# Optimization experiments

Measured on AMD Instinct MI355X. Metric: run time of the kernel, lower is better.

The kernel has to match this reference:

```python
import jax, jax.numpy as jnp
import numpy as np

# Config constants from init_kwargs
DIM_GROUPS = [32, 32]   # hyper_cuts_dim_groups (sum == lsh_key_dim == d_key)
K_MAX = 64              # max candidates kept per query token


def _group_exact_match(qb, kb):
    """qb, kb: [B, L, d] binary {0,1} floats.
    Returns eq[b, i, j] = True iff all d bits of query i equal key j.
    Faithful to merge(Wu-Manber prefix match, Trie full-stride match):
    the Trie stores the full binary vector chunked by stride, so a Trie hit
    requires exact equality of the whole group's bit vector, which subsumes
    the Wu-Manber prefix condition; their intersection is exact equality.
    """
    # number of mismatching bits between query i and key j
    mism = (jnp.einsum('bid,bjd->bij', qb, 1.0 - kb)
            + jnp.einsum('bid,bjd->bij', 1.0 - qb, kb))
    return mism == 0.0


def setup_inputs() -> dict:
    key = jax.random.key(0)
    k1, k2 = jax.random.split(key)
    B, L, D = 4, 2048, 64
    return {
        'query_up': jax.random.normal(k1, (B, L, D), dtype=jnp.float32),
        'key_up': jax.random.normal(k2, (B, L, D), dtype=jnp.float32),
        'head_idx': 0,
    }


def reference(query_up, key_up, head_idx):
    B, L, _ = query_up.shape
    # binary_quantize: (x > 0).float()
    qb = (query_up > 0).astype(jnp.float32)
    kb = (key_up > 0).astype(jnp.float32)
    # per dim-group exact match (Wu-Manber \cap Trie), union across groups
    match = jnp.zeros((B, L, L), dtype=bool)
    start = 0
    for gd in DIM_GROUPS:
        match = match | _group_exact_match(qb[..., start:start + gd],
                                           kb[..., start:start + gd])
        start += gd
    # gather up to K_MAX smallest matching key indices per query, pad with -1
    idx = jnp.where(match, jnp.arange(L, dtype=jnp.int32)[None, None, :], L)
    cand = jnp.sort(idx, axis=-1)[..., :K_MAX]          # [B, L, K_MAX]
    return jnp.where(cand == L, -1, cand)
```

## Files before the change

kernel.cpp:

```cpp
#include <hip/hip_runtime.h>
#include <stdint.h>


#define LSEQ 2048
#define DDIM 64
#define KMAX 64
#define RPW  8

__global__ __launch_bounds__(256) void sig_kernel(
    const float* __restrict__ key, uint2* __restrict__ ksig, int nrows) {
    int wid  = (int)((blockIdx.x * blockDim.x + threadIdx.x) >> 6);
    int lane = threadIdx.x & 63;
    int row0 = wid * RPW;
    if (row0 >= nrows) return;
    const float* base = key + (size_t)row0 * DDIM + lane;
    float v[RPW];
#pragma unroll
    for (int u = 0; u < RPW; ++u)
        v[u] = base[(size_t)u * DDIM];
    unsigned long long m[RPW];
#pragma unroll
    for (int u = 0; u < RPW; ++u)
        m[u] = __ballot(v[u] > 0.0f);
    if (lane == 0) {
#pragma unroll
        for (int u = 0; u < RPW; ++u)
            ksig[row0 + u] = make_uint2((unsigned)m[u], (unsigned)(m[u] >> 32));
    }
}

__global__ __launch_bounds__(256) void match_kernel(
    const float* __restrict__ query, const uint2* __restrict__ ksig,
    int* __restrict__ out, int nq) {
    int wid  = (int)((blockIdx.x * blockDim.x + threadIdx.x) >> 6);
    int lane = threadIdx.x & 63;
    int q0 = wid * 2;
    if (q0 >= nq) return;
    int b = q0 >> 11;

    const float* qp = query + (size_t)q0 * DDIM + lane;
    float v0 = qp[0], v1 = qp[DDIM];
    unsigned long long qm0 = __ballot(v0 > 0.0f);
    unsigned long long qm1 = __ballot(v1 > 0.0f);
    unsigned a0 = (unsigned)qm0, g0 = (unsigned)(qm0 >> 32);
    unsigned a1 = (unsigned)qm1, g1 = (unsigned)(qm1 >> 32);

    const uint4* kt = (const uint4*)(ksig + (size_t)b * LSEQ) + lane;
    unsigned long long acc0 = 0, acc1 = 0;
    int cnt0 = 0, cnt1 = 0;
#pragma unroll
    for (int i = 0; i < LSEQ / 128; ++i) {
        uint4 kv = kt[(size_t)i * 64];
        bool mA0 = (kv.x == a0) | (kv.y == g0);
        bool mB0 = (kv.z == a0) | (kv.w == g0);
        bool mA1 = (kv.x == a1) | (kv.y == g1);
        bool mB1 = (kv.z == a1) | (kv.w == g1);
        unsigned long long s;
        s = __ballot(mA0); acc0 |= s; cnt0 += __popcll(s);
        s = __ballot(mB0); acc0 |= s; cnt0 += __popcll(s);
        s = __ballot(mA1); acc1 |= s; cnt1 += __popcll(s);
        s = __ballot(mB1); acc1 |= s; cnt1 += __popcll(s);
    }

    int* o0 = out + (size_t)q0 * KMAX;
    int* o1 = o0 + KMAX;

    if (acc0 | acc1) {
        const uint2* ks = ksig + (size_t)b * LSEQ;
        unsigned long long below = (1ull << lane) - 1ull;
        for (int t = 0; t < 2; ++t) {
            unsigned qa = t ? a1 : a0, qg = t ? g1 : g0;
            int* ob = t ? o1 : o0;
            int c2 = 0;
            for (int c = 0; c < LSEQ / 64; ++c) {
                uint2 kv = ks[c * 64 + lane];
                bool m = (kv.x == qa) || (kv.y == qg);
                unsigned long long mask = __ballot(m);
                if (m) {
                    int pos = c2 + __popcll(mask & below);
                    if (pos < KMAX) ob[pos] = c * 64 + lane;
                }
                c2 += __popcll(mask);
            }
        }
    }
    if (lane >= cnt0) o0[lane] = -1;
    if (lane >= cnt1) o1[lane] = -1;
}

#define QPB  32
#define NW   16
#define GROUP 32
__global__ __launch_bounds__(1024) void fused_kernel(
    const float* __restrict__ query, const float* __restrict__ key,
    int* __restrict__ out) {
    __shared__ uint2 ks[LSEQ];
    const int bpb  = LSEQ / QPB;
    int b    = blockIdx.x / bpb;
    int qblk = blockIdx.x % bpb;
    int lane = threadIdx.x & 63;
    int wave = threadIdx.x >> 6;
    const float* kb = key + (size_t)b * LSEQ * DDIM;
    for (int g = 0; g < LSEQ / NW / GROUP; ++g) {
        float v[GROUP];
#pragma unroll
        for (int u = 0; u < GROUP; ++u)
            v[u] = kb[(size_t)(g * (NW * GROUP) + u * NW + wave) * DDIM + lane];
        unsigned long long m[GROUP];
#pragma unroll
        for (int u = 0; u < GROUP; ++u) m[u] = __ballot(v[u] > 0.0f);
        if (lane == 0) {
#pragma unroll
            for (int u = 0; u < GROUP; ++u)
                ks[g * (NW * GROUP) + u * NW + wave] =
                    make_uint2((unsigned)m[u], (unsigned)(m[u] >> 32));
        }
    }
    const float* qb = query + ((size_t)b * LSEQ + (size_t)qblk * QPB) * DDIM;
    int q0 = wave * 2;
    float v0 = qb[(size_t)q0 * DDIM + lane];
    float v1 = qb[(size_t)(q0 + 1) * DDIM + lane];
    unsigned long long m0 = __ballot(v0 > 0.0f);
    unsigned long long m1 = __ballot(v1 > 0.0f);
    __syncthreads();
    unsigned long long below = (1ull << lane) - 1ull;
    for (int t = 0; t < 2; ++t) {
        unsigned long long qm = t ? m1 : m0;
        unsigned q1 = (unsigned)qm, q2 = (unsigned)(qm >> 32);
        int* obase = out + ((size_t)b * LSEQ + (size_t)qblk * QPB + q0 + t) * KMAX;
        unsigned long long acc = 0;
        int cnt = 0;
#pragma unroll
        for (int c = 0; c < LSEQ / 64; ++c) {
            uint2 kv = ks[c * 64 + lane];
            bool m = (kv.x == q1) || (kv.y == q2);
            unsigned long long mask = __ballot(m);
            acc |= mask; cnt += __popcll(mask);
        }
        if (acc != 0) {
            int c2 = 0;
            for (int c = 0; c < LSEQ / 64; ++c) {
                uint2 kv = ks[c * 64 + lane];
                bool m = (kv.x == q1) || (kv.y == q2);
                unsigned long long mask = __ballot(m);
                if (m) {
                    int pos = c2 + __popcll(mask & below);
                    if (pos < KMAX) obase[pos] = c * 64 + lane;
                }
                c2 += __popcll(mask);
            }
        }
        if (lane >= cnt) obase[lane] = -1;
    }
}

extern "C" void kernel_launch(void* const* d_in, const int* in_sizes, int n_in,
                              void* d_out, int out_size, void* d_ws, size_t ws_size,
                              hipStream_t stream) {
    const float* q = (const float*)d_in[0];
    const float* k = (const float*)d_in[1];
    int* out = (int*)d_out;

    int total = in_sizes[0];
    int B = total / (LSEQ * DDIM);
    int nrows = B * LSEQ;

    if (ws_size >= (size_t)nrows * sizeof(uint2)) {
        uint2* ksig = (uint2*)d_ws;
        int sig_waves = nrows / RPW;
        sig_kernel<<<sig_waves * 64 / 256, 256, 0, stream>>>(k, ksig, nrows);
        int match_waves = nrows / 2;
        match_kernel<<<match_waves * 64 / 256, 256, 0, stream>>>(q, ksig, out, nrows);
    } else {
        fused_kernel<<<B * (LSEQ / QPB), 1024, 0, stream>>>(q, k, out);
    }
}
```

Measured before the change: 63.29 us.

## Merge signature and match kernels into one cooperative kernel with grid sync

Replaces the two-launch path (key signature kernel, then match kernel) with a single cooperative kernel. Each wave first computes two key signatures, then a grid-wide barrier runs, then the same wave scans and emits matches for two queries. The aim is to remove the second launch and the gap between kernels. In exchange it adds a grid sync, depends on all 256 blocks of 1024 threads being co-resident, and drops the shared-memory fallback path.

```diff
diff --git a/kernel.cpp b/kernel.cpp
--- a/kernel.cpp
+++ b/kernel.cpp
@@ -1,50 +1,18 @@
 #include <hip/hip_runtime.h>
+#include <hip/hip_cooperative_groups.h>
 #include <stdint.h>
+
+namespace cg = cooperative_groups;
 
 
 #define LSEQ 2048
 #define DDIM 64
 #define KMAX 64
-#define RPW  8
 
-__global__ __launch_bounds__(256) void sig_kernel(
-    const float* __restrict__ key, uint2* __restrict__ ksig, int nrows) {
-    int wid  = (int)((blockIdx.x * blockDim.x + threadIdx.x) >> 6);
-    int lane = threadIdx.x & 63;
-    int row0 = wid * RPW;
-    if (row0 >= nrows) return;
-    const float* base = key + (size_t)row0 * DDIM + lane;
-    float v[RPW];
-#pragma unroll
-    for (int u = 0; u < RPW; ++u)
-        v[u] = base[(size_t)u * DDIM];
-    unsigned long long m[RPW];
-#pragma unroll
-    for (int u = 0; u < RPW; ++u)
-        m[u] = __ballot(v[u] > 0.0f);
-    if (lane == 0) {
-#pragma unroll
-        for (int u = 0; u < RPW; ++u)
-            ksig[row0 + u] = make_uint2((unsigned)m[u], (unsigned)(m[u] >> 32));
-    }
-}
-
-__global__ __launch_bounds__(256) void match_kernel(
-    const float* __restrict__ query, const uint2* __restrict__ ksig,
-    int* __restrict__ out, int nq) {
-    int wid  = (int)((blockIdx.x * blockDim.x + threadIdx.x) >> 6);
-    int lane = threadIdx.x & 63;
-    int q0 = wid * 2;
-    if (q0 >= nq) return;
-    int b = q0 >> 11;
-
-    const float* qp = query + (size_t)q0 * DDIM + lane;
-    float v0 = qp[0], v1 = qp[DDIM];
-    unsigned long long qm0 = __ballot(v0 > 0.0f);
-    unsigned long long qm1 = __ballot(v1 > 0.0f);
-    unsigned a0 = (unsigned)qm0, g0 = (unsigned)(qm0 >> 32);
-    unsigned a1 = (unsigned)qm1, g1 = (unsigned)(qm1 >> 32);
-
+__device__ __forceinline__ void scan_and_emit(
+    const uint2* __restrict__ ksig, int b,
+    unsigned a0, unsigned g0, unsigned a1, unsigned g1,
+    int* __restrict__ o0, int* __restrict__ o1, int lane) {
     const uint4* kt = (const uint4*)(ksig + (size_t)b * LSEQ) + lane;
     unsigned long long acc0 = 0, acc1 = 0;
     int cnt0 = 0, cnt1 = 0;
@@ -61,10 +29,6 @@
         s = __ballot(mA1); acc1 |= s; cnt1 += __popcll(s);
         s = __ballot(mB1); acc1 |= s; cnt1 += __popcll(s);
     }
-
-    int* o0 = out + (size_t)q0 * KMAX;
-    int* o1 = o0 + KMAX;
-
     if (acc0 | acc1) {
         const uint2* ks = ksig + (size_t)b * LSEQ;
         unsigned long long below = (1ull << lane) - 1ull;
@@ -88,70 +52,76 @@
     if (lane >= cnt1) o1[lane] = -1;
 }
 
-#define QPB  32
-#define NW   16
-#define GROUP 32
-__global__ __launch_bounds__(1024) void fused_kernel(
+__global__ __launch_bounds__(1024) void coop_kernel(
     const float* __restrict__ query, const float* __restrict__ key,
-    int* __restrict__ out) {
-    __shared__ uint2 ks[LSEQ];
-    const int bpb  = LSEQ / QPB;
-    int b    = blockIdx.x / bpb;
-    int qblk = blockIdx.x % bpb;
+    uint2* __restrict__ ksig, int* __restrict__ out) {
+    int wid  = (int)((blockIdx.x * blockDim.x + threadIdx.x) >> 6);
     int lane = threadIdx.x & 63;
-    int wave = threadIdx.x >> 6;
-    const float* kb = key + (size_t)b * LSEQ * DDIM;
-    for (int g = 0; g < LSEQ / NW / GROUP; ++g) {
-        float v[GROUP];
+
+    int q0 = wid * 2;
+    const float* qp = query + (size_t)q0 * DDIM + lane;
+    float qv0 = qp[0], qv1 = qp[DDIM];
+
+    int r0 = wid * 2;
+    const float* kp = key + (size_t)r0 * DDIM + lane;
+    float kv0 = kp[0], kv1 = kp[DDIM];
+    unsigned long long km0 = __ballot(kv0 > 0.0f);
+    unsigned long long km1 = __ballot(kv1 > 0.0f);
+    if (lane == 0) {
+        ksig[r0]     = make_uint2((unsigned)km0, (unsigned)(km0 >> 32));
+        ksig[r0 + 1] = make_uint2((unsigned)km1, (unsigned)(km1 >> 32));
+    }
+    unsigned long long qm0 = __ballot(qv0 > 0.0f);
+    unsigned long long qm1 = __ballot(qv1 > 0.0f);
+
+    cg::this_grid().sync();
+
+    int b = q0 >> 11;
+    int* o0 = out + (size_t)q0 * KMAX;
+    scan_and_emit(ksig, b,
+                  (unsigned)qm0, (unsigned)(qm0 >> 32),
+                  (unsigned)qm1, (unsigned)(qm1 >> 32),
+                  o0, o0 + KMAX, lane);
+}
+
+#define RPW 8
+__global__ __launch_bounds__(256) void sig_kernel(
+    const float* __restrict__ key, uint2* __restrict__ ksig, int nrows) {
+    int wid  = (int)((blockIdx.x * blockDim.x + threadIdx.x) >> 6);
+    int lane = threadIdx.x & 63;
+    int row0 = wid * RPW;
+    if (row0 >= nrows) return;
+    const float* base = key + (size_t)row0 * DDIM + lane;
+    float v[RPW];
 #pragma unroll
-        for (int u = 0; u < GROUP; ++u)
-            v[u] = kb[(size_t)(g * (NW * GROUP) + u * NW + wave) * DDIM + lane];
-        unsigned long long m[GROUP];
+    for (int u = 0; u < RPW; ++u) v[u] = base[(size_t)u * DDIM];
+    unsigned long long m[RPW];
 #pragma unroll
-        for (int u = 0; u < GROUP; ++u) m[u] = __ballot(v[u] > 0.0f);
-        if (lane == 0) {
+    for (int u = 0; u < RPW; ++u) m[u] = __ballot(v[u] > 0.0f);
+    if (lane == 0) {
 #pragma unroll
-            for (int u = 0; u < GROUP; ++u)
-                ks[g * (NW * GROUP) + u * NW + wave] =
-                    make_uint2((unsigned)m[u], (unsigned)(m[u] >> 32));
-        }
+        for (int u = 0; u < RPW; ++u)
+            ksig[row0 + u] = make_uint2((unsigned)m[u], (unsigned)(m[u] >> 32));
     }
-    const float* qb = query + ((size_t)b * LSEQ + (size_t)qblk * QPB) * DDIM;
-    int q0 = wave * 2;
-    float v0 = qb[(size_t)q0 * DDIM + lane];
-    float v1 = qb[(size_t)(q0 + 1) * DDIM + lane];
-    unsigned long long m0 = __ballot(v0 > 0.0f);
-    unsigned long long m1 = __ballot(v1 > 0.0f);
-    __syncthreads();
-    unsigned long long below = (1ull << lane) - 1ull;
-    for (int t = 0; t < 2; ++t) {
-        unsigned long long qm = t ? m1 : m0;
-        unsigned q1 = (unsigned)qm, q2 = (unsigned)(qm >> 32);
-        int* obase = out + ((size_t)b * LSEQ + (size_t)qblk * QPB + q0 + t) * KMAX;
-        unsigned long long acc = 0;
-        int cnt = 0;
-#pragma unroll
-        for (int c = 0; c < LSEQ / 64; ++c) {
-            uint2 kv = ks[c * 64 + lane];
-            bool m = (kv.x == q1) || (kv.y == q2);
-            unsigned long long mask = __ballot(m);
-            acc |= mask; cnt += __popcll(mask);
-        }
-        if (acc != 0) {
-            int c2 = 0;
-            for (int c = 0; c < LSEQ / 64; ++c) {
-                uint2 kv = ks[c * 64 + lane];
-                bool m = (kv.x == q1) || (kv.y == q2);
-                unsigned long long mask = __ballot(m);
-                if (m) {
-                    int pos = c2 + __popcll(mask & below);
-                    if (pos < KMAX) obase[pos] = c * 64 + lane;
-                }
-                c2 += __popcll(mask);
-            }
-        }
-        if (lane >= cnt) obase[lane] = -1;
-    }
+}
+
+__global__ __launch_bounds__(256) void match_kernel(
+    const float* __restrict__ query, const uint2* __restrict__ ksig,
+    int* __restrict__ out, int nq) {
+    int wid  = (int)((blockIdx.x * blockDim.x + threadIdx.x) >> 6);
+    int lane = threadIdx.x & 63;
+    int q0 = wid * 2;
+    if (q0 >= nq) return;
+    int b = q0 >> 11;
+    const float* qp = query + (size_t)q0 * DDIM + lane;
+    float v0 = qp[0], v1 = qp[DDIM];
+    unsigned long long qm0 = __ballot(v0 > 0.0f);
+    unsigned long long qm1 = __ballot(v1 > 0.0f);
+    int* o0 = out + (size_t)q0 * KMAX;
+    scan_and_emit(ksig, b,
+                  (unsigned)qm0, (unsigned)(qm0 >> 32),
+                  (unsigned)qm1, (unsigned)(qm1 >> 32),
+                  o0, o0 + KMAX, lane);
 }
 
 extern "C" void kernel_launch(void* const* d_in, const int* in_sizes, int n_in,
@@ -165,13 +135,15 @@
     int B = total / (LSEQ * DDIM);
     int nrows = B * LSEQ;
 
-    if (ws_size >= (size_t)nrows * sizeof(uint2)) {
-        uint2* ksig = (uint2*)d_ws;
+    uint2* ksig = (uint2*)d_ws;
+
+    void* args[] = {(void*)&q, (void*)&k, (void*)&ksig, (void*)&out};
+    hipError_t err = hipLaunchCooperativeKernel(
+        (void*)coop_kernel, dim3(B * 64), dim3(1024), args, 0, stream);
+    if (err != hipSuccess) {
         int sig_waves = nrows / RPW;
         sig_kernel<<<sig_waves * 64 / 256, 256, 0, stream>>>(k, ksig, nrows);
         int match_waves = nrows / 2;
         match_kernel<<<match_waves * 64 / 256, 256, 0, stream>>>(q, ksig, out, nrows);
-    } else {
-        fused_kernel<<<B * (LSEQ / QPB), 1024, 0, stream>>>(q, k, out);
     }
 }
```

Result: slower. 100.9 us (+59.5%).

## Fuse signature and match kernels using inter-block flag synchronization per batch

Applied to the files above, without the earlier changes.

Replaces the two-kernel pipeline (key signature kernel, then match kernel) with one kernel. Each block computes key and query signatures for its rows, publishes the key signatures plus a magic flag, and then spin-waits until all 64 blocks of the same batch have published. It then runs the same scan-and-emit. This removes a kernel launch boundary, at the cost of relying on all 64 blocks of a batch being co-resident. It also relies on the flags in the workspace not already holding MAGIC from an earlier call, since nothing resets them, which risks stale reads on repeated launches.

```diff
diff --git a/kernel.cpp b/kernel.cpp
--- a/kernel.cpp
+++ b/kernel.cpp
@@ -5,46 +5,12 @@
 #define LSEQ 2048
 #define DDIM 64
 #define KMAX 64
-#define RPW  8
+#define MAGIC 0x13572468u
 
-__global__ __launch_bounds__(256) void sig_kernel(
-    const float* __restrict__ key, uint2* __restrict__ ksig, int nrows) {
-    int wid  = (int)((blockIdx.x * blockDim.x + threadIdx.x) >> 6);
-    int lane = threadIdx.x & 63;
-    int row0 = wid * RPW;
-    if (row0 >= nrows) return;
-    const float* base = key + (size_t)row0 * DDIM + lane;
-    float v[RPW];
-#pragma unroll
-    for (int u = 0; u < RPW; ++u)
-        v[u] = base[(size_t)u * DDIM];
-    unsigned long long m[RPW];
-#pragma unroll
-    for (int u = 0; u < RPW; ++u)
-        m[u] = __ballot(v[u] > 0.0f);
-    if (lane == 0) {
-#pragma unroll
-        for (int u = 0; u < RPW; ++u)
-            ksig[row0 + u] = make_uint2((unsigned)m[u], (unsigned)(m[u] >> 32));
-    }
-}
-
-__global__ __launch_bounds__(256) void match_kernel(
-    const float* __restrict__ query, const uint2* __restrict__ ksig,
-    int* __restrict__ out, int nq) {
-    int wid  = (int)((blockIdx.x * blockDim.x + threadIdx.x) >> 6);
-    int lane = threadIdx.x & 63;
-    int q0 = wid * 2;
-    if (q0 >= nq) return;
-    int b = q0 >> 11;
-
-    const float* qp = query + (size_t)q0 * DDIM + lane;
-    float v0 = qp[0], v1 = qp[DDIM];
-    unsigned long long qm0 = __ballot(v0 > 0.0f);
-    unsigned long long qm1 = __ballot(v1 > 0.0f);
-    unsigned a0 = (unsigned)qm0, g0 = (unsigned)(qm0 >> 32);
-    unsigned a1 = (unsigned)qm1, g1 = (unsigned)(qm1 >> 32);
-
+__device__ __forceinline__ void scan_and_emit(
+    const uint2* __restrict__ ksig, int b,
+    unsigned a0, unsigned g0, unsigned a1, unsigned g1,
+    int* __restrict__ o0, int* __restrict__ o1, int lane) {
     const uint4* kt = (const uint4*)(ksig + (size_t)b * LSEQ) + lane;
     unsigned long long acc0 = 0, acc1 = 0;
     int cnt0 = 0, cnt1 = 0;
@@ -61,10 +27,6 @@
         s = __ballot(mA1); acc1 |= s; cnt1 += __popcll(s);
         s = __ballot(mB1); acc1 |= s; cnt1 += __popcll(s);
     }
-
-    int* o0 = out + (size_t)q0 * KMAX;
-    int* o1 = o0 + KMAX;
-
     if (acc0 | acc1) {
         const uint2* ks = ksig + (size_t)b * LSEQ;
         unsigned long long below = (1ull << lane) - 1ull;
@@ -86,6 +48,51 @@
     }
     if (lane >= cnt0) o0[lane] = -1;
     if (lane >= cnt1) o1[lane] = -1;
+}
+
+__global__ __launch_bounds__(1024) void cand_kernel(
+    const float* __restrict__ query, const float* __restrict__ key,
+    uint2* __restrict__ ksig, unsigned* __restrict__ flags,
+    int* __restrict__ out) {
+    int wave = threadIdx.x >> 6;
+    int lane = threadIdx.x & 63;
+    int wid  = blockIdx.x * 16 + wave;
+    int r0   = wid * 2;
+
+    const float* kp = key   + (size_t)r0 * DDIM + lane;
+    const float* qp = query + (size_t)r0 * DDIM + lane;
+    float kv0 = kp[0], kv1 = kp[DDIM];
+    float qv0 = qp[0], qv1 = qp[DDIM];
+    unsigned long long km0 = __ballot(kv0 > 0.0f);
+    unsigned long long km1 = __ballot(kv1 > 0.0f);
+    unsigned long long qm0 = __ballot(qv0 > 0.0f);
+    unsigned long long qm1 = __ballot(qv1 > 0.0f);
+
+    if (lane == 0) {
+        unsigned long long* kd = (unsigned long long*)(ksig + r0);
+        __hip_atomic_store(&kd[0], km0, __ATOMIC_RELAXED, __HIP_MEMORY_SCOPE_AGENT);
+        __hip_atomic_store(&kd[1], km1, __ATOMIC_RELAXED, __HIP_MEMORY_SCOPE_AGENT);
+    }
+    __syncthreads();
+    if (threadIdx.x == 0)
+        __hip_atomic_store(&flags[blockIdx.x], MAGIC,
+                           __ATOMIC_RELEASE, __HIP_MEMORY_SCOPE_AGENT);
+
+    const unsigned* gf = flags + (blockIdx.x & ~63);
+    for (;;) {
+        unsigned f = __hip_atomic_load(&gf[lane],
+                                       __ATOMIC_RELAXED, __HIP_MEMORY_SCOPE_AGENT);
+        if (__ballot(f == MAGIC) == ~0ull) break;
+        __builtin_amdgcn_s_sleep(1);
+    }
+    __builtin_amdgcn_fence(__ATOMIC_ACQUIRE, "agent");
+
+    int b = r0 >> 11;
+    int* o0 = out + (size_t)r0 * KMAX;
+    scan_and_emit(ksig, b,
+                  (unsigned)qm0, (unsigned)(qm0 >> 32),
+                  (unsigned)qm1, (unsigned)(qm1 >> 32),
+                  o0, o0 + KMAX, lane);
 }
 
 #define QPB  32
@@ -165,12 +172,12 @@
     int B = total / (LSEQ * DDIM);
     int nrows = B * LSEQ;
 
-    if (ws_size >= (size_t)nrows * sizeof(uint2)) {
-        uint2* ksig = (uint2*)d_ws;
-        int sig_waves = nrows / RPW;
-        sig_kernel<<<sig_waves * 64 / 256, 256, 0, stream>>>(k, ksig, nrows);
-        int match_waves = nrows / 2;
-        match_kernel<<<match_waves * 64 / 256, 256, 0, stream>>>(q, ksig, out, nrows);
+    size_t sig_bytes  = (size_t)nrows * sizeof(uint2);
+    size_t need       = sig_bytes + (size_t)(B * 64) * sizeof(unsigned);
+    if (ws_size >= need) {
+        uint2*    ksig  = (uint2*)d_ws;
+        unsigned* flags = (unsigned*)((char*)d_ws + sig_bytes);
+        cand_kernel<<<B * 64, 1024, 0, stream>>>(q, k, ksig, flags, out);
     } else {
         fused_kernel<<<B * (LSEQ / QPB), 1024, 0, stream>>>(q, k, out);
     }
```

Measured after the change: 98.26 us. 55.2% more time.
